# Kernel tuning notes

Hardware: AMD Instinct MI355X
Metric: run time of the kernel (lower is better)

## Reference

```python
import jax, jax.numpy as jnp
import numpy as np

B, S, D, H = 2, 2048, 1024, 16
DK = D // H


def setup_inputs() -> dict:
    key = jax.random.key(0)
    ks = jax.random.split(key, 8)
    scale = 1.0 / np.sqrt(D)
    inp = {
        "query": jax.random.normal(ks[0], (B, S, D), dtype=jnp.float32),
        "key": jax.random.normal(ks[1], (B, S, D), dtype=jnp.float32),
        "value": jax.random.normal(ks[2], (B, S, D), dtype=jnp.float32),
        # causal mask, broadcastable over batch and heads
        "mask": jnp.tril(jnp.ones((S, S), dtype=jnp.int32))[None, None, :, :],
        "W_q": jax.random.normal(ks[3], (D, D), dtype=jnp.float32) * scale,
        "W_k": jax.random.normal(ks[4], (D, D), dtype=jnp.float32) * scale,
        "W_v": jax.random.normal(ks[5], (D, D), dtype=jnp.float32) * scale,
        "W_o": jax.random.normal(ks[6], (D, D), dtype=jnp.float32) * scale,
    }
    return inp


def _split_heads(t):
    Bb, Ss, _ = t.shape
    return t.reshape(Bb, Ss, H, DK).transpose(0, 2, 1, 3)  # [B,H,S,DK]


def reference(query, key, value, mask, W_q, W_k, W_v, W_o):
    # Linear(d,d,bias=False): y = x @ W^T (torch stores weight as [out,in])
    Q = _split_heads(query @ W_q.T)
    K = _split_heads(key @ W_k.T)
    V = _split_heads(value @ W_v.T)
    scores = jnp.einsum("bhqd,bhkd->bhqk", Q, K) / jnp.sqrt(jnp.float32(DK))
    scores = jnp.where(mask == 0, -jnp.inf, scores)
    weights = jax.nn.softmax(scores, axis=-1)
    weights = jnp.nan_to_num(weights, nan=0.0)  # fully-masked rows -> 0
    # dropout is identity at inference
    x = jnp.einsum("bhqk,bhkd->bhqd", weights, V)
    x = x.transpose(0, 2, 1, 3).reshape(B, S, D)
    return x @ W_o.T
```

## Files before the change

### kernel.cpp

```cpp
#include <hip/hip_runtime.h>
#include <hip/hip_bf16.h>

#define D_MODEL 1024
#define NHEAD   16
#define HDK     64
#define SEQ     2048
#define BATCH   2
#define BS      (BATCH * SEQ)

typedef __attribute__((ext_vector_type(8))) short bf16x8;
typedef __attribute__((ext_vector_type(4))) float f32x4;

__device__ __forceinline__ unsigned short f2bf(float f) {
    unsigned u = __builtin_bit_cast(unsigned, f);
    u += 0x7fffu + ((u >> 16) & 1u);
    return (unsigned short)(u >> 16);
}

typedef const void __attribute__((address_space(1))) gas_void;
typedef void __attribute__((address_space(3))) las_void;

__device__ __forceinline__ void gll16(const void* g, void* l) {
    __builtin_amdgcn_global_load_lds((gas_void*)g, (las_void*)l, 16, 0, 0);
}

__device__ __forceinline__ void cast_body(const float* __restrict__ src,
                                          unsigned short* __restrict__ dst, int i) {
    const float4* p = (const float4*)src + (size_t)i * 2;
    float4 a = p[0], b = p[1];
    ushort4 lo = make_ushort4(f2bf(a.x), f2bf(a.y), f2bf(a.z), f2bf(a.w));
    ushort4 hi = make_ushort4(f2bf(b.x), f2bf(b.y), f2bf(b.z), f2bf(b.w));
    ushort4* q = (ushort4*)dst + (size_t)i * 2;
    q[0] = lo; q[1] = hi;
}

__global__ __launch_bounds__(256)
void cast_act(const float* a, const float* b, const float* c,
              unsigned short* oa, unsigned short* ob, unsigned short* oc, int n8) {
    int i = blockIdx.x * 256 + threadIdx.x;
    if (i >= n8) return;
    const float* s = blockIdx.y == 0 ? a : blockIdx.y == 1 ? b : c;
    unsigned short* d = blockIdx.y == 0 ? oa : blockIdx.y == 1 ? ob : oc;
    cast_body(s, d, i);
}

__global__ __launch_bounds__(256)
void cast_wt(const float* a, const float* b, const float* c, const float* dd,
             unsigned short* oa, unsigned short* ob, unsigned short* oc, unsigned short* od, int n8) {
    int i = blockIdx.x * 256 + threadIdx.x;
    if (i >= n8) return;
    const float* s = blockIdx.y == 0 ? a : blockIdx.y == 1 ? b : blockIdx.y == 2 ? c : dd;
    unsigned short* d = blockIdx.y == 0 ? oa : blockIdx.y == 1 ? ob : blockIdx.y == 2 ? oc : od;
    cast_body(s, d, i);
}

__device__ __forceinline__ void gemm_kloop128(const unsigned short* __restrict__ X,
                                              const unsigned short* __restrict__ W,
                                              unsigned short* As, unsigned short* Bs,
                                              int bm, int bn, f32x4 acc[4][4]) {
    const int t    = threadIdx.x;
    const int w    = t >> 6;
    const int L    = t & 63;
    const int quad = L >> 4;
    const int lm   = L & 15;
    const int r8   = L >> 3;
    const int sl   = L & 7;
    const int xcol = ((sl ^ r8) & 7) * 8;
    const int wr   = (w >> 1) * 64;
    const int wc   = (w & 1) * 64;

    for (int kt = 0; kt < D_MODEL; kt += 64) {
        __syncthreads();
        #pragma unroll
        for (int i = 0; i < 4; ++i) {
            int c = w * 4 + i;
            gll16(X + (size_t)(bm + c * 8 + r8) * D_MODEL + kt + xcol, &As[c * 512]);
        }
        #pragma unroll
        for (int i = 0; i < 4; ++i) {
            int c = w * 4 + i;
            gll16(W + (size_t)(bn + c * 8 + r8) * D_MODEL + kt + xcol, &Bs[c * 512]);
        }
        __syncthreads();

        #pragma unroll
        for (int ch = 0; ch < 2; ++ch) {
            bf16x8 af[4], bfr[4];
            #pragma unroll
            for (int ms = 0; ms < 4; ++ms) {
                int row = wr + ms * 16 + lm;
                af[ms] = *(const bf16x8*)&As[row * 64 + (((ch * 4 + quad) ^ (row & 7)) * 8)];
            }
            #pragma unroll
            for (int ns = 0; ns < 4; ++ns) {
                int row = wc + ns * 16 + lm;
                bfr[ns] = *(const bf16x8*)&Bs[row * 64 + (((ch * 4 + quad) ^ (row & 7)) * 8)];
            }
            #pragma unroll
            for (int ms = 0; ms < 4; ++ms)
                #pragma unroll
                for (int ns = 0; ns < 4; ++ns)
                    acc[ms][ns] = __builtin_amdgcn_mfma_f32_16x16x32_bf16(
                        af[ms], bfr[ns], acc[ms][ns], 0, 0, 0);
        }
    }
}

__global__ __launch_bounds__(256, 3)
void proj_gemm(const unsigned short* __restrict__ qx, const unsigned short* __restrict__ kx,
               const unsigned short* __restrict__ vx, const unsigned short* __restrict__ wq,
               const unsigned short* __restrict__ wk, const unsigned short* __restrict__ wv,
               unsigned short* __restrict__ Qp, unsigned short* __restrict__ Kp,
               unsigned short* __restrict__ VT) {
    __shared__ __align__(16) unsigned short As[128 * 64];
    __shared__ __align__(16) unsigned short Bs[128 * 64];

    const int p = blockIdx.z;
    const unsigned short* X = p == 0 ? qx : p == 1 ? kx : vx;
    const unsigned short* W = p == 0 ? wq : p == 1 ? wk : wv;
    const int bm = blockIdx.y * 128, bn = blockIdx.x * 128;

    f32x4 acc[4][4];
    #pragma unroll
    for (int ms = 0; ms < 4; ++ms)
        #pragma unroll
        for (int ns = 0; ns < 4; ++ns)
            acc[ms][ns] = (f32x4){0.f, 0.f, 0.f, 0.f};

    gemm_kloop128(X, W, As, Bs, bm, bn, acc);

    const int t = threadIdx.x, w = t >> 6, L = t & 63, quad = L >> 4, lm = L & 15;
    const int wr = (w >> 1) * 64, wc = (w & 1) * 64;
    if (p == 2) {
        const int b   = bm >> 11;
        const int s_in = (bm & (SEQ - 1)) + wr;
        #pragma unroll
        for (int ms = 0; ms < 4; ++ms)
            #pragma unroll
            for (int ns = 0; ns < 4; ++ns) {
                int dg = bn + wc + ns * 16 + lm;
                int h  = dg >> 6, d = dg & 63;
                ushort4 pk = make_ushort4(f2bf(acc[ms][ns][0]), f2bf(acc[ms][ns][1]),
                                          f2bf(acc[ms][ns][2]), f2bf(acc[ms][ns][3]));
                *(ushort4*)&VT[((size_t)((b * NHEAD + h) * HDK + d)) * SEQ +
                               s_in + ms * 16 + quad * 4] = pk;
            }
    } else {
        unsigned short* Y = p == 0 ? Qp : Kp;
        const float scl = p == 0 ? 0.125f : 1.0f;
        #pragma unroll
        for (int ms = 0; ms < 4; ++ms)
            #pragma unroll
            for (int ns = 0; ns < 4; ++ns)
                #pragma unroll
                for (int r = 0; r < 4; ++r)
                    Y[(size_t)(bm + wr + ms * 16 + quad * 4 + r) * D_MODEL +
                      bn + wc + ns * 16 + lm] = f2bf(acc[ms][ns][r] * scl);
    }
}

__global__ __launch_bounds__(256, 3)
void out_gemm(const unsigned short* __restrict__ X, const unsigned short* __restrict__ W,
              float* __restrict__ Y) {
    __shared__ __align__(16) unsigned short As[128 * 64];
    __shared__ __align__(16) unsigned short Bs[128 * 64];
    const int bm = blockIdx.y * 128, bn = blockIdx.x * 128;

    f32x4 acc[4][4];
    #pragma unroll
    for (int ms = 0; ms < 4; ++ms)
        #pragma unroll
        for (int ns = 0; ns < 4; ++ns)
            acc[ms][ns] = (f32x4){0.f, 0.f, 0.f, 0.f};

    gemm_kloop128(X, W, As, Bs, bm, bn, acc);

    const int t = threadIdx.x, w = t >> 6, L = t & 63, quad = L >> 4, lm = L & 15;
    const int wr = (w >> 1) * 64, wc = (w & 1) * 64;
    #pragma unroll
    for (int ms = 0; ms < 4; ++ms)
        #pragma unroll
        for (int ns = 0; ns < 4; ++ns)
            #pragma unroll
            for (int r = 0; r < 4; ++r)
                Y[(size_t)(bm + wr + ms * 16 + quad * 4 + r) * D_MODEL +
                  bn + wc + ns * 16 + lm] = acc[ms][ns][r];
}

__global__ __launch_bounds__(256, 5)
void attn_mfma(const unsigned short* __restrict__ Q, const unsigned short* __restrict__ K,
               const unsigned short* __restrict__ VT, unsigned short* __restrict__ A) {
    __shared__ __align__(16) unsigned short Ks[64 * 72];
    __shared__ __align__(16) unsigned short Vs[64 * 72];
    __shared__ __align__(16) unsigned short Ps[4 * 16 * 72];

    const int t    = threadIdx.x;
    const int w    = t >> 6;
    const int L    = t & 63;
    const int quad = L >> 4;
    const int lm   = L & 15;
    const int qt   = 31 - blockIdx.x;
    const int h    = blockIdx.y;
    const int b    = blockIdx.z;
    const int q0   = qt * 64;
    const size_t hb  = (size_t)b * SEQ * D_MODEL + h * HDK;
    const size_t vhb = (size_t)(b * NHEAD + h) * HDK;

    const int qrow = q0 + w * 16 + lm;

    bf16x8 Qf0, Qf1;
    {
        const unsigned short* qp = Q + hb + (size_t)qrow * D_MODEL + quad * 8;
        Qf0 = *(const bf16x8*)qp;
        Qf1 = *(const bf16x8*)(qp + 32);
    }

    f32x4 Oacc[4];
    #pragma unroll
    for (int nt = 0; nt < 4; ++nt) Oacc[nt] = (f32x4){0.f, 0.f, 0.f, 0.f};
    float m_run = -INFINITY, l_run = 0.f;

    const int srow = t >> 2;
    const int c0   = t & 3;
    const unsigned short* kp = K + hb + (size_t)srow * D_MODEL + c0 * 16;
    const unsigned short* vp = VT + (vhb + srow) * SEQ + c0 * 16;

    float4 k0r = *(const float4*)kp;
    float4 k1r = *(const float4*)(kp + 8);
    float4 v0r = *(const float4*)vp;
    float4 v1r = *(const float4*)(vp + 8);

    unsigned short* ps = &Ps[w * 16 * 72];

    for (int kt = 0; kt <= qt; ++kt) {
        const int k0 = kt * 64;
        __syncthreads();
        *(float4*)&Ks[srow * 72 + c0 * 16]     = k0r;
        *(float4*)&Ks[srow * 72 + c0 * 16 + 8] = k1r;
        *(float4*)&Vs[srow * 72 + c0 * 16]     = v0r;
        *(float4*)&Vs[srow * 72 + c0 * 16 + 8] = v1r;
        if (kt < qt) {
            k0r = *(const float4*)(kp + (size_t)(k0 + 64) * D_MODEL);
            k1r = *(const float4*)(kp + (size_t)(k0 + 64) * D_MODEL + 8);
            v0r = *(const float4*)(vp + k0 + 64);
            v1r = *(const float4*)(vp + k0 + 64 + 8);
        }
        __syncthreads();

        f32x4 S[4];
        #pragma unroll
        for (int ct = 0; ct < 4; ++ct) {
            bf16x8 a0 = *(const bf16x8*)&Ks[(ct * 16 + lm) * 72 + quad * 8];
            bf16x8 a1 = *(const bf16x8*)&Ks[(ct * 16 + lm) * 72 + 32 + quad * 8];
            f32x4 z = (f32x4){0.f, 0.f, 0.f, 0.f};
            z = __builtin_amdgcn_mfma_f32_16x16x32_bf16(a0, Qf0, z, 0, 0, 0);
            z = __builtin_amdgcn_mfma_f32_16x16x32_bf16(a1, Qf1, z, 0, 0, 0);
            S[ct] = z;
        }

        if (k0 + 63 > q0 + w * 16) {
            #pragma unroll
            for (int ct = 0; ct < 4; ++ct)
                #pragma unroll
                for (int r = 0; r < 4; ++r)
                    if ((k0 + ct * 16 + quad * 4 + r) > qrow)
                        S[ct][r] = -1e30f;
        }

        float m = fmaxf(fmaxf(fmaxf(S[0][0], S[0][1]), fmaxf(S[0][2], S[0][3])),
                        fmaxf(fmaxf(S[1][0], S[1][1]), fmaxf(S[1][2], S[1][3])));
        m = fmaxf(m, fmaxf(fmaxf(fmaxf(S[2][0], S[2][1]), fmaxf(S[2][2], S[2][3])),
                           fmaxf(fmaxf(S[3][0], S[3][1]), fmaxf(S[3][2], S[3][3]))));
        m = fmaxf(m, __shfl_xor(m, 16));
        m = fmaxf(m, __shfl_xor(m, 32));
        const float m_new = fmaxf(m_run, m);
        const float alpha = __expf(m_run - m_new);
        m_run = m_new;
        float psum = 0.f;
        #pragma unroll
        for (int ct = 0; ct < 4; ++ct)
            #pragma unroll
            for (int r = 0; r < 4; ++r) {
                float e = __expf(S[ct][r] - m_new);
                S[ct][r] = e;
                psum += e;
            }
        psum += __shfl_xor(psum, 16);
        psum += __shfl_xor(psum, 32);
        l_run = l_run * alpha + psum;

        #pragma unroll
        for (int ct = 0; ct < 4; ++ct) {
            ushort4 pk = make_ushort4(f2bf(S[ct][0]), f2bf(S[ct][1]),
                                      f2bf(S[ct][2]), f2bf(S[ct][3]));
            *(ushort4*)&ps[lm * 72 + ct * 16 + quad * 4] = pk;
        }
        bf16x8 Pb0 = *(const bf16x8*)&ps[lm * 72 + quad * 8];
        bf16x8 Pb1 = *(const bf16x8*)&ps[lm * 72 + 32 + quad * 8];

        #pragma unroll
        for (int nt = 0; nt < 4; ++nt) {
            bf16x8 a0 = *(const bf16x8*)&Vs[(nt * 16 + lm) * 72 + quad * 8];
            bf16x8 a1 = *(const bf16x8*)&Vs[(nt * 16 + lm) * 72 + 32 + quad * 8];
            f32x4 o = Oacc[nt];
            #pragma unroll
            for (int r = 0; r < 4; ++r) o[r] *= alpha;
            o = __builtin_amdgcn_mfma_f32_16x16x32_bf16(a0, Pb0, o, 0, 0, 0);
            o = __builtin_amdgcn_mfma_f32_16x16x32_bf16(a1, Pb1, o, 0, 0, 0);
            Oacc[nt] = o;
        }
    }

    const float inv_l = 1.f / l_run;
    #pragma unroll
    for (int nt = 0; nt < 4; ++nt) {
        ushort4 pk = make_ushort4(f2bf(Oacc[nt][0] * inv_l), f2bf(Oacc[nt][1] * inv_l),
                                  f2bf(Oacc[nt][2] * inv_l), f2bf(Oacc[nt][3] * inv_l));
        *(ushort4*)&ps[lm * 72 + nt * 16 + quad * 4] = pk;
    }
    #pragma unroll
    for (int p = 0; p < 2; ++p) {
        int qr = p * 8 + (L >> 3);
        int dc = (L & 7) * 8;
        uint4 val = *(const uint4*)&ps[qr * 72 + dc];
        *(uint4*)&A[hb + (size_t)(q0 + w * 16 + qr) * D_MODEL + dc] = val;
    }
}

extern "C" void kernel_launch(void* const* d_in, const int* in_sizes, int n_in,
                              void* d_out, int out_size, void* d_ws, size_t ws_size,
                              hipStream_t stream) {
    const float* q  = (const float*)d_in[0];
    const float* k  = (const float*)d_in[1];
    const float* v  = (const float*)d_in[2];
    const float* Wq = (const float*)d_in[4];
    const float* Wk = (const float*)d_in[5];
    const float* Wv = (const float*)d_in[6];
    const float* Wo = (const float*)d_in[7];
    float* out = (float*)d_out;

    char* ws = (char*)d_ws;
    const size_t MB = 1024 * 1024;
    unsigned short* qb  = (unsigned short*)(ws + 0 * MB);
    unsigned short* kb  = (unsigned short*)(ws + 8 * MB);
    unsigned short* vb  = (unsigned short*)(ws + 16 * MB);
    unsigned short* wqb = (unsigned short*)(ws + 24 * MB);
    unsigned short* wkb = (unsigned short*)(ws + 26 * MB);
    unsigned short* wvb = (unsigned short*)(ws + 28 * MB);
    unsigned short* wob = (unsigned short*)(ws + 30 * MB);
    unsigned short* Qp  = (unsigned short*)(ws + 32 * MB);
    unsigned short* Kp  = (unsigned short*)(ws + 40 * MB);
    unsigned short* VTp = (unsigned short*)(ws + 48 * MB);
    unsigned short* Ap  = (unsigned short*)(ws + 56 * MB);

    const int nX8 = BS * D_MODEL / 8;
    const int nW8 = D_MODEL * D_MODEL / 8;
    cast_act<<<dim3(nX8 / 256, 3), 256, 0, stream>>>(q, k, v, qb, kb, vb, nX8);
    cast_wt <<<dim3(nW8 / 256, 4), 256, 0, stream>>>(Wq, Wk, Wv, Wo, wqb, wkb, wvb, wob, nW8);

    proj_gemm<<<dim3(D_MODEL / 128, BS / 128, 3), 256, 0, stream>>>(
        qb, kb, vb, wqb, wkb, wvb, Qp, Kp, VTp);

    attn_mfma<<<dim3(SEQ / 64, NHEAD, BATCH), 256, 0, stream>>>(Qp, Kp, VTp, Ap);

    out_gemm<<<dim3(D_MODEL / 128, BS / 128), 256, 0, stream>>>(Ap, wob, out);
}
```

Before: 249.7 us.

## Pair causal query tiles per attention block, double-buffer K/V, shrink out_gemm tiles

Each attention block now handles two query tiles, i and 31-i, so every block does an equal share of the causal work. The grid is halved to 16 blocks in x. K/V staging moves to double-buffered LDS with one barrier per iteration instead of two, and bf16 packing of P uses a perm (truncation instead of round-to-nearest). out_gemm switches to 128x64 tiles to double the block count on the small output GEMM. These changes add LDS use and lower the attention occupancy hint, and the truncation slightly changes numerics.

New measurement: 225.9 us. 1.11x faster.

```diff
diff --git a/kernel.cpp b/kernel.cpp
--- a/kernel.cpp
+++ b/kernel.cpp
@@ -15,6 +15,11 @@
     unsigned u = __builtin_bit_cast(unsigned, f);
     u += 0x7fffu + ((u >> 16) & 1u);
     return (unsigned short)(u >> 16);
+}
+
+__device__ __forceinline__ unsigned pack_hi(float x, float y) {
+    return __builtin_amdgcn_perm(__builtin_bit_cast(unsigned, y),
+                                 __builtin_bit_cast(unsigned, x), 0x07060302u);
 }
 
 typedef const void __attribute__((address_space(1))) gas_void;
@@ -106,6 +111,56 @@
     }
 }
 
+__device__ __forceinline__ void gemm_kloop64(const unsigned short* __restrict__ X,
+                                             const unsigned short* __restrict__ W,
+                                             unsigned short* As, unsigned short* Bs,
+                                             int bm, int bn, f32x4 acc[2][4]) {
+    const int t    = threadIdx.x;
+    const int w    = t >> 6;
+    const int L    = t & 63;
+    const int quad = L >> 4;
+    const int lm   = L & 15;
+    const int r8   = L >> 3;
+    const int sl   = L & 7;
+    const int xcol = ((sl ^ r8) & 7) * 8;
+
+    for (int kt = 0; kt < D_MODEL; kt += 64) {
+        __syncthreads();
+        #pragma unroll
+        for (int i = 0; i < 4; ++i) {
+            int c = w * 4 + i;
+            gll16(X + (size_t)(bm + c * 8 + r8) * D_MODEL + kt + xcol, &As[c * 512]);
+        }
+        #pragma unroll
+        for (int i = 0; i < 2; ++i) {
+            int c = w * 2 + i;
+            gll16(W + (size_t)(bn + c * 8 + r8) * D_MODEL + kt + xcol, &Bs[c * 512]);
+        }
+        __syncthreads();
+
+        #pragma unroll
+        for (int ch = 0; ch < 2; ++ch) {
+            bf16x8 af[2], bfr[4];
+            #pragma unroll
+            for (int ms = 0; ms < 2; ++ms) {
+                int row = w * 32 + ms * 16 + lm;
+                af[ms] = *(const bf16x8*)&As[row * 64 + (((ch * 4 + quad) ^ (row & 7)) * 8)];
+            }
+            #pragma unroll
+            for (int ns = 0; ns < 4; ++ns) {
+                int row = ns * 16 + lm;
+                bfr[ns] = *(const bf16x8*)&Bs[row * 64 + (((ch * 4 + quad) ^ (row & 7)) * 8)];
+            }
+            #pragma unroll
+            for (int ms = 0; ms < 2; ++ms)
+                #pragma unroll
+                for (int ns = 0; ns < 4; ++ns)
+                    acc[ms][ns] = __builtin_amdgcn_mfma_f32_16x16x32_bf16(
+                        af[ms], bfr[ns], acc[ms][ns], 0, 0, 0);
+        }
+    }
+}
+
 __global__ __launch_bounds__(256, 3)
 void proj_gemm(const unsigned short* __restrict__ qx, const unsigned short* __restrict__ kx,
                const unsigned short* __restrict__ vx, const unsigned short* __restrict__ wq,
@@ -132,7 +187,7 @@
     const int t = threadIdx.x, w = t >> 6, L = t & 63, quad = L >> 4, lm = L & 15;
     const int wr = (w >> 1) * 64, wc = (w & 1) * 64;
     if (p == 2) {
-        const int b   = bm >> 11;
+        const int b    = bm >> 11;
         const int s_in = (bm & (SEQ - 1)) + wr;
         #pragma unroll
         for (int ms = 0; ms < 4; ++ms)
@@ -159,39 +214,38 @@
     }
 }
 
-__global__ __launch_bounds__(256, 3)
+__global__ __launch_bounds__(256)
 void out_gemm(const unsigned short* __restrict__ X, const unsigned short* __restrict__ W,
               float* __restrict__ Y) {
     __shared__ __align__(16) unsigned short As[128 * 64];
-    __shared__ __align__(16) unsigned short Bs[128 * 64];
-    const int bm = blockIdx.y * 128, bn = blockIdx.x * 128;
-
-    f32x4 acc[4][4];
+    __shared__ __align__(16) unsigned short Bs[64 * 64];
+    const int bm = blockIdx.y * 128, bn = blockIdx.x * 64;
+
+    f32x4 acc[2][4];
     #pragma unroll
-    for (int ms = 0; ms < 4; ++ms)
+    for (int ms = 0; ms < 2; ++ms)
         #pragma unroll
         for (int ns = 0; ns < 4; ++ns)
             acc[ms][ns] = (f32x4){0.f, 0.f, 0.f, 0.f};
 
-    gemm_kloop128(X, W, As, Bs, bm, bn, acc);
+    gemm_kloop64(X, W, As, Bs, bm, bn, acc);
 
     const int t = threadIdx.x, w = t >> 6, L = t & 63, quad = L >> 4, lm = L & 15;
-    const int wr = (w >> 1) * 64, wc = (w & 1) * 64;
     #pragma unroll
-    for (int ms = 0; ms < 4; ++ms)
+    for (int ms = 0; ms < 2; ++ms)
         #pragma unroll
         for (int ns = 0; ns < 4; ++ns)
             #pragma unroll
             for (int r = 0; r < 4; ++r)
-                Y[(size_t)(bm + wr + ms * 16 + quad * 4 + r) * D_MODEL +
-                  bn + wc + ns * 16 + lm] = acc[ms][ns][r];
-}
-
-__global__ __launch_bounds__(256, 5)
+                Y[(size_t)(bm + w * 32 + ms * 16 + quad * 4 + r) * D_MODEL +
+                  bn + ns * 16 + lm] = acc[ms][ns][r];
+}
+
+__global__ __launch_bounds__(256, 3)
 void attn_mfma(const unsigned short* __restrict__ Q, const unsigned short* __restrict__ K,
                const unsigned short* __restrict__ VT, unsigned short* __restrict__ A) {
-    __shared__ __align__(16) unsigned short Ks[64 * 72];
-    __shared__ __align__(16) unsigned short Vs[64 * 72];
+    __shared__ __align__(16) unsigned short Ks[2][64 * 72];
+    __shared__ __align__(16) unsigned short Vs[2][64 * 72];
     __shared__ __align__(16) unsigned short Ps[4 * 16 * 72];
 
     const int t    = threadIdx.x;
@@ -199,131 +253,151 @@
     const int L    = t & 63;
     const int quad = L >> 4;
     const int lm   = L & 15;
-    const int qt   = 31 - blockIdx.x;
     const int h    = blockIdx.y;
     const int b    = blockIdx.z;
-    const int q0   = qt * 64;
     const size_t hb  = (size_t)b * SEQ * D_MODEL + h * HDK;
     const size_t vhb = (size_t)(b * NHEAD + h) * HDK;
 
-    const int qrow = q0 + w * 16 + lm;
-
-    bf16x8 Qf0, Qf1;
-    {
-        const unsigned short* qp = Q + hb + (size_t)qrow * D_MODEL + quad * 8;
-        Qf0 = *(const bf16x8*)qp;
-        Qf1 = *(const bf16x8*)(qp + 32);
-    }
-
-    f32x4 Oacc[4];
-    #pragma unroll
-    for (int nt = 0; nt < 4; ++nt) Oacc[nt] = (f32x4){0.f, 0.f, 0.f, 0.f};
-    float m_run = -INFINITY, l_run = 0.f;
-
     const int srow = t >> 2;
-    const int c0   = t & 3;
-    const unsigned short* kp = K + hb + (size_t)srow * D_MODEL + c0 * 16;
-    const unsigned short* vp = VT + (vhb + srow) * SEQ + c0 * 16;
-
-    float4 k0r = *(const float4*)kp;
-    float4 k1r = *(const float4*)(kp + 8);
-    float4 v0r = *(const float4*)vp;
-    float4 v1r = *(const float4*)(vp + 8);
-
+    const int sc   = (t & 3) * 16;
+    const unsigned short* kp = K + hb + (size_t)srow * D_MODEL + sc;
+    const unsigned short* vp = VT + (vhb + srow) * SEQ + sc;
     unsigned short* ps = &Ps[w * 16 * 72];
 
-    for (int kt = 0; kt <= qt; ++kt) {
-        const int k0 = kt * 64;
+    for (int half = 0; half < 2; ++half) {
+        const int qt   = half ? 31 - (int)blockIdx.x : (int)blockIdx.x;
+        const int q0   = qt * 64;
+        const int qrow = q0 + w * 16 + lm;
+
+        bf16x8 Qf0, Qf1;
+        {
+            const unsigned short* qp = Q + hb + (size_t)qrow * D_MODEL + quad * 8;
+            Qf0 = *(const bf16x8*)qp;
+            Qf1 = *(const bf16x8*)(qp + 32);
+        }
+
+        f32x4 Oacc[4];
+        #pragma unroll
+        for (int nt = 0; nt < 4; ++nt) Oacc[nt] = (f32x4){0.f, 0.f, 0.f, 0.f};
+        float m_run = -INFINITY, l_run = 0.f;
+
+        float4 kr0 = *(const float4*)kp;
+        float4 kr1 = *(const float4*)(kp + 8);
+        float4 vr0 = *(const float4*)vp;
+        float4 vr1 = *(const float4*)(vp + 8);
+        *(float4*)&Ks[0][srow * 72 + sc]     = kr0;
+        *(float4*)&Ks[0][srow * 72 + sc + 8] = kr1;
+        *(float4*)&Vs[0][srow * 72 + sc]     = vr0;
+        *(float4*)&Vs[0][srow * 72 + sc + 8] = vr1;
+        if (qt >= 1) {
+            kr0 = *(const float4*)(kp + (size_t)64 * D_MODEL);
+            kr1 = *(const float4*)(kp + (size_t)64 * D_MODEL + 8);
+            vr0 = *(const float4*)(vp + 64);
+            vr1 = *(const float4*)(vp + 64 + 8);
+        }
         __syncthreads();
-        *(float4*)&Ks[srow * 72 + c0 * 16]     = k0r;
-        *(float4*)&Ks[srow * 72 + c0 * 16 + 8] = k1r;
-        *(float4*)&Vs[srow * 72 + c0 * 16]     = v0r;
-        *(float4*)&Vs[srow * 72 + c0 * 16 + 8] = v1r;
-        if (kt < qt) {
-            k0r = *(const float4*)(kp + (size_t)(k0 + 64) * D_MODEL);
-            k1r = *(const float4*)(kp + (size_t)(k0 + 64) * D_MODEL + 8);
-            v0r = *(const float4*)(vp + k0 + 64);
-            v1r = *(const float4*)(vp + k0 + 64 + 8);
-        }
-        __syncthreads();
-
-        f32x4 S[4];
-        #pragma unroll
-        for (int ct = 0; ct < 4; ++ct) {
-            bf16x8 a0 = *(const bf16x8*)&Ks[(ct * 16 + lm) * 72 + quad * 8];
-            bf16x8 a1 = *(const bf16x8*)&Ks[(ct * 16 + lm) * 72 + 32 + quad * 8];
-            f32x4 z = (f32x4){0.f, 0.f, 0.f, 0.f};
-            z = __builtin_amdgcn_mfma_f32_16x16x32_bf16(a0, Qf0, z, 0, 0, 0);
-            z = __builtin_amdgcn_mfma_f32_16x16x32_bf16(a1, Qf1, z, 0, 0, 0);
-            S[ct] = z;
-        }
-
-        if (k0 + 63 > q0 + w * 16) {
+
+        int bb = 0;
+        for (int kt = 0; kt <= qt; ++kt) {
+            const int k0 = kt * 64;
+            const unsigned short* Kc = Ks[bb];
+            const unsigned short* Vc = Vs[bb];
+            if (kt < qt) {
+                unsigned short* Kn = Ks[bb ^ 1];
+                unsigned short* Vn = Vs[bb ^ 1];
+                *(float4*)&Kn[srow * 72 + sc]     = kr0;
+                *(float4*)&Kn[srow * 72 + sc + 8] = kr1;
+                *(float4*)&Vn[srow * 72 + sc]     = vr0;
+                *(float4*)&Vn[srow * 72 + sc + 8] = vr1;
+                if (kt + 2 <= qt) {
+                    kr0 = *(const float4*)(kp + (size_t)(k0 + 128) * D_MODEL);
+                    kr1 = *(const float4*)(kp + (size_t)(k0 + 128) * D_MODEL + 8);
+                    vr0 = *(const float4*)(vp + k0 + 128);
+                    vr1 = *(const float4*)(vp + k0 + 128 + 8);
+                }
+            }
+
+            f32x4 S[4];
+            #pragma unroll
+            for (int ct = 0; ct < 4; ++ct) {
+                bf16x8 a0 = *(const bf16x8*)&Kc[(ct * 16 + lm) * 72 + quad * 8];
+                bf16x8 a1 = *(const bf16x8*)&Kc[(ct * 16 + lm) * 72 + 32 + quad * 8];
+                f32x4 z = (f32x4){0.f, 0.f, 0.f, 0.f};
+                z = __builtin_amdgcn_mfma_f32_16x16x32_bf16(a0, Qf0, z, 0, 0, 0);
+                z = __builtin_amdgcn_mfma_f32_16x16x32_bf16(a1, Qf1, z, 0, 0, 0);
+                S[ct] = z;
+            }
+
+            if (k0 + 63 > q0 + w * 16) {
+                #pragma unroll
+                for (int ct = 0; ct < 4; ++ct)
+                    #pragma unroll
+                    for (int r = 0; r < 4; ++r)
+                        if ((k0 + ct * 16 + quad * 4 + r) > qrow)
+                            S[ct][r] = -1e30f;
+            }
+
+            float m = fmaxf(fmaxf(fmaxf(S[0][0], S[0][1]), fmaxf(S[0][2], S[0][3])),
+                            fmaxf(fmaxf(S[1][0], S[1][1]), fmaxf(S[1][2], S[1][3])));
+            m = fmaxf(m, fmaxf(fmaxf(fmaxf(S[2][0], S[2][1]), fmaxf(S[2][2], S[2][3])),
+                               fmaxf(fmaxf(S[3][0], S[3][1]), fmaxf(S[3][2], S[3][3]))));
+            m = fmaxf(m, __shfl_xor(m, 16));
+            m = fmaxf(m, __shfl_xor(m, 32));
+            const float m_new = fmaxf(m_run, m);
+            const float alpha = __expf(m_run - m_new);
+            m_run = m_new;
+            float psum = 0.f;
             #pragma unroll
             for (int ct = 0; ct < 4; ++ct)
                 #pragma unroll
-                for (int r = 0; r < 4; ++r)
-                    if ((k0 + ct * 16 + quad * 4 + r) > qrow)
-                        S[ct][r] = -1e30f;
-        }
-
-        float m = fmaxf(fmaxf(fmaxf(S[0][0], S[0][1]), fmaxf(S[0][2], S[0][3])),
-                        fmaxf(fmaxf(S[1][0], S[1][1]), fmaxf(S[1][2], S[1][3])));
-        m = fmaxf(m, fmaxf(fmaxf(fmaxf(S[2][0], S[2][1]), fmaxf(S[2][2], S[2][3])),
-                           fmaxf(fmaxf(S[3][0], S[3][1]), fmaxf(S[3][2], S[3][3]))));
-        m = fmaxf(m, __shfl_xor(m, 16));
-        m = fmaxf(m, __shfl_xor(m, 32));
-        const float m_new = fmaxf(m_run, m);
-        const float alpha = __expf(m_run - m_new);
-        m_run = m_new;
-        float psum = 0.f;
-        #pragma unroll
-        for (int ct = 0; ct < 4; ++ct)
-            #pragma unroll
-            for (int r = 0; r < 4; ++r) {
-                float e = __expf(S[ct][r] - m_new);
-                S[ct][r] = e;
-                psum += e;
-            }
-        psum += __shfl_xor(psum, 16);
-        psum += __shfl_xor(psum, 32);
-        l_run = l_run * alpha + psum;
-
-        #pragma unroll
-        for (int ct = 0; ct < 4; ++ct) {
-            ushort4 pk = make_ushort4(f2bf(S[ct][0]), f2bf(S[ct][1]),
-                                      f2bf(S[ct][2]), f2bf(S[ct][3]));
-            *(ushort4*)&ps[lm * 72 + ct * 16 + quad * 4] = pk;
-        }
-        bf16x8 Pb0 = *(const bf16x8*)&ps[lm * 72 + quad * 8];
-        bf16x8 Pb1 = *(const bf16x8*)&ps[lm * 72 + 32 + quad * 8];
-
+                for (int r = 0; r < 4; ++r) {
+                    float e = __expf(S[ct][r] - m_new);
+                    S[ct][r] = e;
+                    psum += e;
+                }
+            psum += __shfl_xor(psum, 16);
+            psum += __shfl_xor(psum, 32);
+            l_run = l_run * alpha + psum;
+
+            #pragma unroll
+            for (int ct = 0; ct < 4; ++ct) {
+                uint2 pw = make_uint2(pack_hi(S[ct][0], S[ct][1]),
+                                      pack_hi(S[ct][2], S[ct][3]));
+                *(uint2*)&ps[lm * 72 + ct * 16 + quad * 4] = pw;
+            }
+            bf16x8 Pb0 = *(const bf16x8*)&ps[lm * 72 + quad * 8];
+            bf16x8 Pb1 = *(const bf16x8*)&ps[lm * 72 + 32 + quad * 8];
+
+            #pragma unroll
+            for (int nt = 0; nt < 4; ++nt) {
+                bf16x8 a0 = *(const bf16x8*)&Vc[(nt * 16 + lm) * 72 + quad * 8];
+                bf16x8 a1 = *(const bf16x8*)&Vc[(nt * 16 + lm) * 72 + 32 + quad * 8];
+                f32x4 o = Oacc[nt];
+                #pragma unroll
+                for (int r = 0; r < 4; ++r) o[r] *= alpha;
+                o = __builtin_amdgcn_mfma_f32_16x16x32_bf16(a0, Pb0, o, 0, 0, 0);
+                o = __builtin_amdgcn_mfma_f32_16x16x32_bf16(a1, Pb1, o, 0, 0, 0);
+                Oacc[nt] = o;
+            }
+
+            __syncthreads();
+            bb ^= 1;
+        }
+
+        const float inv_l = 1.f / l_run;
         #pragma unroll
         for (int nt = 0; nt < 4; ++nt) {
-            bf16x8 a0 = *(const bf16x8*)&Vs[(nt * 16 + lm) * 72 + quad * 8];
-            bf16x8 a1 = *(const bf16x8*)&Vs[(nt * 16 + lm) * 72 + 32 + quad * 8];
-            f32x4 o = Oacc[nt];
-            #pragma unroll
-            for (int r = 0; r < 4; ++r) o[r] *= alpha;
-            o = __builtin_amdgcn_mfma_f32_16x16x32_bf16(a0, Pb0, o, 0, 0, 0);
-            o = __builtin_amdgcn_mfma_f32_16x16x32_bf16(a1, Pb1, o, 0, 0, 0);
-            Oacc[nt] = o;
-        }
-    }
-
-    const float inv_l = 1.f / l_run;
-    #pragma unroll
-    for (int nt = 0; nt < 4; ++nt) {
-        ushort4 pk = make_ushort4(f2bf(Oacc[nt][0] * inv_l), f2bf(Oacc[nt][1] * inv_l),
-                                  f2bf(Oacc[nt][2] * inv_l), f2bf(Oacc[nt][3] * inv_l));
-        *(ushort4*)&ps[lm * 72 + nt * 16 + quad * 4] = pk;
-    }
-    #pragma unroll
-    for (int p = 0; p < 2; ++p) {
-        int qr = p * 8 + (L >> 3);
-        int dc = (L & 7) * 8;
-        uint4 val = *(const uint4*)&ps[qr * 72 + dc];
-        *(uint4*)&A[hb + (size_t)(q0 + w * 16 + qr) * D_MODEL + dc] = val;
+            ushort4 pk = make_ushort4(f2bf(Oacc[nt][0] * inv_l), f2bf(Oacc[nt][1] * inv_l),
+                                      f2bf(Oacc[nt][2] * inv_l), f2bf(Oacc[nt][3] * inv_l));
+            *(ushort4*)&ps[lm * 72 + nt * 16 + quad * 4] = pk;
+        }
+        #pragma unroll
+        for (int p = 0; p < 2; ++p) {
+            int qr = p * 8 + (L >> 3);
+            int dc = (L & 7) * 8;
+            uint4 val = *(const uint4*)&ps[qr * 72 + dc];
+            *(uint4*)&A[hb + (size_t)(q0 + w * 16 + qr) * D_MODEL + dc] = val;
+        }
     }
 }
 
@@ -361,7 +435,7 @@
     proj_gemm<<<dim3(D_MODEL / 128, BS / 128, 3), 256, 0, stream>>>(
         qb, kb, vb, wqb, wkb, wvb, Qp, Kp, VTp);
 
-    attn_mfma<<<dim3(SEQ / 64, NHEAD, BATCH), 256, 0, stream>>>(Qp, Kp, VTp, Ap);
-
-    out_gemm<<<dim3(D_MODEL / 128, BS / 128), 256, 0, stream>>>(Ap, wob, out);
-}
+    attn_mfma<<<dim3(16, NHEAD, BATCH), 256, 0, stream>>>(Qp, Kp, VTp, Ap);
+
+    out_gemm<<<dim3(D_MODEL / 64, BS / 128), 256, 0, stream>>>(Ap, wob, out);
+}
```
